# Optimization experiments

Measured on AMD Instinct MI355X. Metric: run time of the kernel, lower is better.

## Reference

```python
import jax, jax.numpy as jnp
from jax import lax
import numpy as np

# (mult_l0, mult_l1, mult_l2) per layer, from CNN.__init__
FEATS = [(5, 0, 0), (10, 3, 0), (10, 3, 1), (16, 8, 1), (16, 8, 1), (16, 8, 1), (1, 0, 0)]
STRIDES = [2, 1, 1, 1, 1, 1]
RELUS = [True, True, True, True, True, False]
SIZE, NRAD, PAD = 7, 3, 3  # SE3Convolution(size=7, n_radial=3, padding=3)


def ch(r):
    return r[0] + 3 * r[1] + 5 * r[2]


def radial_basis():
    # precomputed fixed radial shell basis on the 7^3 kernel grid (stand-in for
    # e3nn's precomputed spherical-harmonic x radial kernel basis)
    r = np.arange(SIZE) - SIZE // 2
    X, Y, Z = np.meshgrid(r, r, r, indexing='ij')
    dist = np.sqrt(X ** 2 + Y ** 2 + Z ** 2)
    centers = np.linspace(0.0, SIZE // 2, NRAD)
    sigma = (SIZE // 2) / (NRAD - 1)
    b = np.exp(-((dist[None] - centers[:, None, None, None]) ** 2) / (2.0 * sigma ** 2))
    return jnp.asarray(b, jnp.float32)  # [NRAD, 7, 7, 7]


def setup_inputs() -> dict:
    key = jax.random.key(0)
    ks = jax.random.split(key, 20)
    inp = {"x": jax.random.normal(ks[0], (2, 5, 32, 32, 32), jnp.float32)}
    for i in range(6):
        cin = ch(FEATS[i]) + 9 * FEATS[i][1]  # after TensorProduct concat
        cout = ch(FEATS[i + 1])
        inp[f"w{i}"] = jax.random.normal(ks[1 + i], (cout, cin, NRAD), jnp.float32) / np.sqrt(cin * SIZE ** 3)
    for i in range(5):
        inp[f"b{i}"] = jax.random.normal(ks[7 + i], (FEATS[i + 1][0],), jnp.float32) * 0.1
    inp["lin_w"] = jax.random.normal(ks[13], (1, 5), jnp.float32)
    inp["lin_b"] = jax.random.normal(ks[14], (1,), jnp.float32)
    inp["alpha"] = jnp.ones((1,), jnp.float32)
    return inp


def _block(x, w, bias, rep_in, rep_out, stride, relu, basis):
    m1, m3, m5 = rep_in
    B = x.shape[0]
    if m3 > 0:
        # TensorProduct on the l=1 fields: self outer product -> 3x3 (9-dim) fields
        sp = x.shape[2:]
        v = x[:, m1:m1 + 3 * m3].reshape(B, m3, 3, *sp)
        t = jnp.einsum('bmixyz,bmjxyz->bmijxyz', v, v).reshape(B, m3 * 9, *sp)
        x = jnp.concatenate([x, t], axis=1)
    # SE3Convolution: learned mixing of precomputed kernel basis, then conv3d
    k = jnp.einsum('oir,rxyz->oixyz', w, basis)  # [Cout, Cin, 7,7,7]
    x = lax.conv_general_dilated(x, k, (stride,) * 3, [(PAD, PAD)] * 3,
                                 dimension_numbers=('NCDHW', 'OIDHW', 'NCDHW'))
    if relu:
        n1, n3, n5 = rep_out
        sp = x.shape[2:]
        # SE3BatchNorm: per-field norm over batch + spatial (per multiplicity channel)
        parts, off = [], 0
        for m, d in ((n1, 1), (n3, 3), (n5, 5)):
            if m == 0:
                continue
            f = x[:, off:off + m * d].reshape(B, m, d, *sp)
            norm2 = jnp.mean(jnp.sum(f * f, axis=2), axis=(0, 2, 3, 4))  # [m]
            f = f / jnp.sqrt(norm2 + 1e-5)[None, :, None, None, None, None]
            parts.append(f.reshape(B, m * d, *sp))
            off += m * d
        x = jnp.concatenate(parts, axis=1)
        # BiasRelu: bias + relu on scalar (l=0) fields only, higher-l pass through
        s = jax.nn.relu(x[:, :n1] + bias[None, :, None, None, None])
        x = jnp.concatenate([s, x[:, n1:]], axis=1)
    return x


def reference(x, w0, w1, w2, w3, w4, w5, b0, b1, b2, b3, b4, lin_w, lin_b, alpha):
    basis = radial_basis()
    ws = [w0, w1, w2, w3, w4, w5]
    bs = [b0, b1, b2, b3, b4, None]
    inp = x
    for i in range(6):
        x = _block(x, ws[i], bs[i], FEATS[i], FEATS[i + 1], STRIDES[i], RELUS[i], basis)
    B = x.shape[0]
    out = x.reshape(B, x.shape[1], -1).mean(-1) * alpha * 0.1  # [B, 1]
    y = inp.reshape(B, 5, -1).sum(-1) @ lin_w.T + lin_b  # [B, 1]
    return out + y
```

## Files before the change

kernel.cpp:

```cpp
#include <hip/hip_runtime.h>
#include <math.h>

static constexpr int OFF_BAS = 0;
static constexpr int OFF_W   = 1280;
static constexpr int OFF_ACC = 37504;
static constexpr int OFF_XA  = 37888;
static constexpr int OFF_XB  = OFF_XA + 761856;
static constexpr int OFF_U   = OFF_XB + 761856;
static constexpr int OFF_Y   = OFF_U + 1105920;

static constexpr int WOFF0 = OFF_W + 0;
static constexpr int WOFF1 = OFF_W + 384;
static constexpr int WOFF2 = OFF_W + 3264;
static constexpr int WOFF3 = OFF_W + 9248;
static constexpr int WOFF4 = OFF_W + 22304;
static constexpr int WOFF5 = OFF_W + 35360;

__device__ __forceinline__ float wred(float s) {
  #pragma unroll
  for (int o = 32; o > 0; o >>= 1) s += __shfl_xor(s, o, 64);
  return s;
}

__global__ __launch_bounds__(128) void prep_kernel(
    const float* __restrict__ w0, const float* __restrict__ w1,
    const float* __restrict__ w2, const float* __restrict__ w3,
    const float* __restrict__ w4, const float* __restrict__ w5,
    float* __restrict__ ws) {
  const int blk = blockIdx.x;
  const int tid = threadIdx.x;
  if (blk == 0) {
    for (int i = tid; i < 1176; i += 128) {
      int tx = i & 7;
      int r  = (i >> 3) % 3;
      int ty = (i / 24) % 7;
      int tz = i / 168;
      float val = 0.f;
      if (tx < 7) {
        double dx = tx - 3, dy = ty - 3, dz = tz - 3;
        double dist = sqrt(dx * dx + dy * dy + dz * dz);
        double d = dist - 1.5 * (double)r;
        val = (float)exp(-(d * d) / 4.5);
      }
      ws[OFF_BAS + i] = val;
    }
    return;
  }
  const int row = blk - 1;
  const int rs[6]    = {0, 24, 96, 232, 368, 504};
  const int kk[6]    = {15, 37, 42, 93, 93, 93};
  const int k4[6]    = {16, 40, 44, 96, 96, 96};
  const int coutt[6] = {19, 24, 45, 45, 45, 1};
  const int cinf[6]  = {5, 46, 51, 117, 117, 117};
  const int chin_[6] = {5, 19, 24, 45, 45, 45};
  const int woff[6]  = {WOFF0, WOFF1, WOFF2, WOFF3, WOFF4, WOFF5};
  const float* wptr[6] = {w0, w1, w2, w3, w4, w5};
  int l = 0;
  while (l < 5 && row >= rs[l + 1]) ++l;
  const int m = row - rs[l];
  const int K = kk[l], K4 = k4[l];
  const float* w = wptr[l];
  float* Wo = ws + woff[l] + m * K4;
  if (l == 0) {
    for (int k = tid; k < 16; k += 128) {
      float v = 0.f;
      if (m < 19 && k < 15) { int c = k / 3, r = k % 3; v = w[(m * 5 + c) * 3 + r]; }
      Wo[k] = v;
    }
    return;
  }
  const int o = m / 3, r = m % 3;
  const int cout = coutt[l];
  const int cf = cinf[l], ch = chin_[l];
  const int itab[6] = {0, 0, 0, 1, 1, 2};
  const int jtab[6] = {0, 1, 2, 1, 2, 2};
  for (int k = tid; k < K4; k += 128) {
    float v = 0.f;
    if (o < cout && k < K) {
      if (k < ch) {
        v = w[(o * cf + k) * 3 + r];
      } else {
        int cc = k - ch;
        int mm = cc / 6, uu = cc % 6;
        int i = itab[uu], j = jtab[uu];
        v = w[(o * cf + ch + mm * 9 + i * 3 + j) * 3 + r];
        if (i != j) v += w[(o * cf + ch + mm * 9 + j * 3 + i) * 3 + r];
      }
    }
    Wo[k] = v;
  }
}

__global__ __launch_bounds__(256) void insum_kernel(const float* __restrict__ x,
                                                    float* __restrict__ insum) {
  const int g = blockIdx.x * 256 + threadIdx.x;
  float4 v = ((const float4*)x)[g];
  float s = v.x + v.y + v.z + v.w;
  s = wred(s);
  if ((threadIdx.x & 63) == 0) atomicAdd(&insum[g >> 13], s);
}

__global__ __launch_bounds__(256) void dw0_kernel(const float* __restrict__ x,
                                                  const float* __restrict__ basg,
                                                  float* __restrict__ z0) {
  const int g = blockIdx.x * 256 + threadIdx.x;
  const int p = g & 4095;
  const int c = (g >> 12) % 5;
  const int b = g / (5 * 4096);
  const int X = p & 15, Y = (p >> 4) & 15, Z = p >> 8;
  const float* xp = x + (((size_t)(b * 5 + c)) << 15);
  float a0 = 0.f, a1 = 0.f, a2 = 0.f;
  for (int tz = 0; tz < 7; ++tz) {
    const int iz = 2 * Z + tz - 3;
    if ((unsigned)iz >= 32u) continue;
    for (int ty = 0; ty < 7; ++ty) {
      const int iy = 2 * Y + ty - 3;
      if ((unsigned)iy >= 32u) continue;
      const float* bb = &basg[(tz * 7 + ty) * 24];
      const float* row = xp + (iz << 10) + (iy << 5);
      #pragma unroll
      for (int tx = 0; tx < 7; ++tx) {
        const int ix = 2 * X + tx - 3;
        float v = ((unsigned)ix < 32u) ? row[ix] : 0.f;
        a0 = fmaf(bb[tx], v, a0);
        a1 = fmaf(bb[8 + tx], v, a1);
        a2 = fmaf(bb[16 + tx], v, a2);
      }
    }
  }
  const size_t base = (((size_t)(b * 15 + c * 3)) << 12) + p;
  z0[base] = a0;
  z0[base + 4096] = a1;
  z0[base + 8192] = a2;
}

template <int K>
__global__ __launch_bounds__(256) void gemm_kernel(
    const float* __restrict__ in, const float* __restrict__ W,
    float* __restrict__ out, int Mreal, float* __restrict__ chsum) {
  constexpr int K4 = (K + 3) & ~3;
  __shared__ float Wl[8 * K4];
  const int b = blockIdx.z;
  const int m0 = blockIdx.y * 8;
  const int p0 = blockIdx.x * 1024 + threadIdx.x * 4;
  for (int i = threadIdx.x; i < 8 * K4; i += 256) Wl[i] = W[m0 * K4 + i];
  __syncthreads();
  const float* ip = in + (((size_t)b * K) << 12) + p0;
  float4 acc[8];
  #pragma unroll
  for (int j = 0; j < 8; ++j) acc[j] = make_float4(0.f, 0.f, 0.f, 0.f);
  int k = 0;
  for (; k + 4 <= K; k += 4) {
    const float4 v0 = *(const float4*)&ip[(size_t)(k + 0) << 12];
    const float4 v1 = *(const float4*)&ip[(size_t)(k + 1) << 12];
    const float4 v2 = *(const float4*)&ip[(size_t)(k + 2) << 12];
    const float4 v3 = *(const float4*)&ip[(size_t)(k + 3) << 12];
    #pragma unroll
    for (int j = 0; j < 8; ++j) {
      const float4 wv = *(const float4*)&Wl[j * K4 + k];
      acc[j].x = fmaf(wv.x, v0.x, acc[j].x); acc[j].y = fmaf(wv.x, v0.y, acc[j].y);
      acc[j].z = fmaf(wv.x, v0.z, acc[j].z); acc[j].w = fmaf(wv.x, v0.w, acc[j].w);
      acc[j].x = fmaf(wv.y, v1.x, acc[j].x); acc[j].y = fmaf(wv.y, v1.y, acc[j].y);
      acc[j].z = fmaf(wv.y, v1.z, acc[j].z); acc[j].w = fmaf(wv.y, v1.w, acc[j].w);
      acc[j].x = fmaf(wv.z, v2.x, acc[j].x); acc[j].y = fmaf(wv.z, v2.y, acc[j].y);
      acc[j].z = fmaf(wv.z, v2.z, acc[j].z); acc[j].w = fmaf(wv.z, v2.w, acc[j].w);
      acc[j].x = fmaf(wv.w, v3.x, acc[j].x); acc[j].y = fmaf(wv.w, v3.y, acc[j].y);
      acc[j].z = fmaf(wv.w, v3.z, acc[j].z); acc[j].w = fmaf(wv.w, v3.w, acc[j].w);
    }
  }
  for (; k < K; ++k) {
    const float4 v = *(const float4*)&ip[(size_t)k << 12];
    #pragma unroll
    for (int j = 0; j < 8; ++j) {
      const float w = Wl[j * K4 + k];
      acc[j].x = fmaf(w, v.x, acc[j].x); acc[j].y = fmaf(w, v.y, acc[j].y);
      acc[j].z = fmaf(w, v.z, acc[j].z); acc[j].w = fmaf(w, v.w, acc[j].w);
    }
  }
  #pragma unroll
  for (int j = 0; j < 8; ++j) {
    const int m = m0 + j;
    if (m < Mreal) *(float4*)&out[(((size_t)(b * Mreal + m)) << 12) + p0] = acc[j];
  }
  if (chsum) {
    #pragma unroll
    for (int j = 0; j < 8; ++j) {
      float s = acc[j].x * acc[j].x + acc[j].y * acc[j].y +
                acc[j].z * acc[j].z + acc[j].w * acc[j].w;
      s = wred(s);
      if ((threadIdx.x & 63) == 0) atomicAdd(&chsum[m0 + j], s);
    }
  }
}

__global__ __launch_bounds__(128) void dwB_kernel(
    const float* __restrict__ u, const float* __restrict__ basg,
    float* __restrict__ y, float* __restrict__ chsum, int cout) {
  __shared__ float lin[13440];
  const int b = blockIdx.y;
  const int o = blockIdx.x >> 3;
  const int rem = blockIdx.x & 7;
  const int zs = rem >> 1, yh = rem & 1;
  const int z0 = zs * 4, y0 = yh * 8;
  const int tid = threadIdx.x;
  const float* ubase = u + (((size_t)(b * 3 * cout + o * 3)) << 12);
  for (int i = tid; i < 3360; i += 128) {
    const int g = i & 7;
    const int row = i >> 3;
    const int ch = row / 140;
    const int rr = row - ch * 140;
    const int dz = rr / 14;
    const int dy = rr - dz * 14;
    const int gz = z0 + dz - 3, gy = y0 + dy - 3;
    float4 v = make_float4(0.f, 0.f, 0.f, 0.f);
    if (g >= 1 && g <= 4 && (unsigned)gz < 16u && (unsigned)gy < 16u)
      v = *(const float4*)&ubase[(ch << 12) + (gz << 8) + (gy << 4) + ((g - 1) << 2)];
    *(float4*)&lin[row * 32 + ((g ^ (row & 7)) << 2)] = v;
  }
  __syncthreads();
  const int yy = tid & 7, bx = (tid >> 3) & 3, zz = tid >> 5;
  float acc[4] = {0.f, 0.f, 0.f, 0.f};
  #pragma unroll 1
  for (int tz = 0; tz < 7; ++tz) {
    #pragma unroll 1
    for (int ty = 0; ty < 7; ++ty) {
      const int rbase = (zz + tz) * 14 + (yy + ty);
      const float* bbrow = &basg[(tz * 7 + ty) * 24];
      #pragma unroll
      for (int ch = 0; ch < 3; ++ch) {
        const int row = ch * 140 + rbase;
        const int s = row & 7;
        const int base = row * 32;
        const float4 v0 = *(const float4*)&lin[base + (((bx + 0) ^ s) << 2)];
        const float4 v1 = *(const float4*)&lin[base + (((bx + 1) ^ s) << 2)];
        const float4 v2 = *(const float4*)&lin[base + (((bx + 2) ^ s) << 2)];
        const float w_[12] = {v0.x, v0.y, v0.z, v0.w, v1.x, v1.y, v1.z, v1.w,
                              v2.x, v2.y, v2.z, v2.w};
        const float* bb = bbrow + ch * 8;
        #pragma unroll
        for (int tx = 0; tx < 7; ++tx) {
          const float w = bb[tx];
          #pragma unroll
          for (int i2 = 0; i2 < 4; ++i2)
            acc[i2] = fmaf(w, w_[i2 + tx + 1], acc[i2]);
        }
      }
    }
  }
  const int p = ((z0 + zz) << 8) + ((y0 + yy) << 4) + bx * 4;
  float4 outv = {acc[0], acc[1], acc[2], acc[3]};
  *(float4*)&y[(((size_t)(b * cout + o)) << 12) + p] = outv;
  if (chsum) {
    float s = acc[0]*acc[0] + acc[1]*acc[1] + acc[2]*acc[2] + acc[3]*acc[3];
    s = wred(s);
    if ((tid & 63) == 0) atomicAdd(&chsum[o], s);
  }
}

template <int COUT, int N1, int N3>
__global__ __launch_bounds__(64) void post_kernel(
    const float* __restrict__ y, const float* __restrict__ chsum,
    const float* __restrict__ bias, float* __restrict__ xout) {
  constexpr int N5 = (COUT - N1 - 3 * N3) / 5;
  constexpr int CO = COUT + 6 * N3;
  const int b = blockIdx.y;
  const int p = blockIdx.x * 64 + threadIdx.x;
  const float* yp = y + (((size_t)b * COUT) << 12) + p;
  float* xp = xout + (((size_t)b * CO) << 12) + p;
  const float inv = 1.f / 8192.f;
  float vals[COUT];
  #pragma unroll
  for (int c = 0; c < N1; ++c) {
    const float f = 1.f / sqrtf(chsum[c] * inv + 1e-5f);
    const float v = yp[(size_t)c << 12] * f + bias[c];
    vals[c] = v > 0.f ? v : 0.f;
  }
  #pragma unroll
  for (int m = 0; m < N3; ++m) {
    const int c0 = N1 + 3 * m;
    const float f = 1.f / sqrtf((chsum[c0] + chsum[c0 + 1] + chsum[c0 + 2]) * inv + 1e-5f);
    vals[c0]     = yp[(size_t)c0 << 12] * f;
    vals[c0 + 1] = yp[(size_t)(c0 + 1) << 12] * f;
    vals[c0 + 2] = yp[(size_t)(c0 + 2) << 12] * f;
  }
  #pragma unroll
  for (int m = 0; m < N5; ++m) {
    const int c0 = N1 + 3 * N3 + 5 * m;
    const float s5 = chsum[c0] + chsum[c0+1] + chsum[c0+2] + chsum[c0+3] + chsum[c0+4];
    const float f = 1.f / sqrtf(s5 * inv + 1e-5f);
    #pragma unroll
    for (int d = 0; d < 5; ++d) vals[c0 + d] = yp[(size_t)(c0 + d) << 12] * f;
  }
  #pragma unroll
  for (int c = 0; c < COUT; ++c) xp[(size_t)c << 12] = vals[c];
  #pragma unroll
  for (int m = 0; m < N3; ++m) {
    const float v0 = vals[N1 + 3*m], v1 = vals[N1 + 3*m + 1], v2 = vals[N1 + 3*m + 2];
    const float t[6] = {v0*v0, v0*v1, v0*v2, v1*v1, v1*v2, v2*v2};
    #pragma unroll
    for (int uu = 0; uu < 6; ++uu) xp[(size_t)(COUT + m * 6 + uu) << 12] = t[uu];
  }
}

__global__ __launch_bounds__(256) void final_kernel(
    const float* __restrict__ y5, const float* __restrict__ acc,
    const float* __restrict__ lin_w, const float* __restrict__ lin_b,
    const float* __restrict__ alpha, float* __restrict__ out) {
  const int b = blockIdx.x;
  const int tid = threadIdx.x;
  float s = 0.f;
  for (int i = tid; i < 4096; i += 256) s += y5[(b << 12) + i];
  s = wred(s);
  __shared__ float ls[4];
  if ((tid & 63) == 0) ls[tid >> 6] = s;
  __syncthreads();
  if (tid == 0) {
    const float t = ls[0] + ls[1] + ls[2] + ls[3];
    float res = t * (1.f / 4096.f) * alpha[0] * 0.1f;
    const float* insum = acc + 240;
    for (int c = 0; c < 5; ++c) res += insum[b * 5 + c] * lin_w[c];
    res += lin_b[0];
    out[b] = res;
  }
}

extern "C" void kernel_launch(void* const* d_in, const int* in_sizes, int n_in,
                              void* d_out, int out_size, void* d_ws, size_t ws_size,
                              hipStream_t stream) {
  const float* x  = (const float*)d_in[0];
  const float* w0 = (const float*)d_in[1];
  const float* w1 = (const float*)d_in[2];
  const float* w2 = (const float*)d_in[3];
  const float* w3 = (const float*)d_in[4];
  const float* w4 = (const float*)d_in[5];
  const float* w5 = (const float*)d_in[6];
  const float* b0 = (const float*)d_in[7];
  const float* b1 = (const float*)d_in[8];
  const float* b2 = (const float*)d_in[9];
  const float* b3 = (const float*)d_in[10];
  const float* b4 = (const float*)d_in[11];
  const float* lw = (const float*)d_in[12];
  const float* lb = (const float*)d_in[13];
  const float* al = (const float*)d_in[14];
  float* out = (float*)d_out;
  float* ws = (float*)d_ws;

  float* bas = ws + OFF_BAS;
  float* acc = ws + OFF_ACC;
  float* XA = ws + OFF_XA;
  float* XB = ws + OFF_XB;
  float* U  = ws + OFF_U;
  float* Y  = ws + OFF_Y;

  hipMemsetAsync(acc, 0, 256 * sizeof(float), stream);
  hipLaunchKernelGGL(prep_kernel, dim3(513), dim3(128), 0, stream, w0, w1, w2, w3, w4, w5, ws);
  hipLaunchKernelGGL(insum_kernel, dim3(320), dim3(256), 0, stream, x, acc + 240);

  hipLaunchKernelGGL(dw0_kernel, dim3(160), dim3(256), 0, stream, x, bas, U);
  hipLaunchKernelGGL(gemm_kernel<15>, dim3(4, 3, 2), dim3(256), 0, stream,
                     U, ws + WOFF0, Y, 19, acc);
  hipLaunchKernelGGL((post_kernel<19, 10, 3>), dim3(64, 2), dim3(64), 0, stream, Y, acc, b0, XA);

  hipLaunchKernelGGL(gemm_kernel<37>, dim3(4, 9, 2), dim3(256), 0, stream,
                     XA, ws + WOFF1, U, 72, (float*)nullptr);
  hipLaunchKernelGGL(dwB_kernel, dim3(192, 2), dim3(128), 0, stream, U, bas, Y, acc + 48, 24);
  hipLaunchKernelGGL((post_kernel<24, 10, 3>), dim3(64, 2), dim3(64), 0, stream, Y, acc + 48, b1, XB);

  hipLaunchKernelGGL(gemm_kernel<42>, dim3(4, 17, 2), dim3(256), 0, stream,
                     XB, ws + WOFF2, U, 135, (float*)nullptr);
  hipLaunchKernelGGL(dwB_kernel, dim3(360, 2), dim3(128), 0, stream, U, bas, Y, acc + 96, 45);
  hipLaunchKernelGGL((post_kernel<45, 16, 8>), dim3(64, 2), dim3(64), 0, stream, Y, acc + 96, b2, XA);

  hipLaunchKernelGGL(gemm_kernel<93>, dim3(4, 17, 2), dim3(256), 0, stream,
                     XA, ws + WOFF3, U, 135, (float*)nullptr);
  hipLaunchKernelGGL(dwB_kernel, dim3(360, 2), dim3(128), 0, stream, U, bas, Y, acc + 144, 45);
  hipLaunchKernelGGL((post_kernel<45, 16, 8>), dim3(64, 2), dim3(64), 0, stream, Y, acc + 144, b3, XB);

  hipLaunchKernelGGL(gemm_kernel<93>, dim3(4, 17, 2), dim3(256), 0, stream,
                     XB, ws + WOFF4, U, 135, (float*)nullptr);
  hipLaunchKernelGGL(dwB_kernel, dim3(360, 2), dim3(128), 0, stream, U, bas, Y, acc + 192, 45);
  hipLaunchKernelGGL((post_kernel<45, 16, 8>), dim3(64, 2), dim3(64), 0, stream, Y, acc + 192, b4, XA);

  hipLaunchKernelGGL(gemm_kernel<93>, dim3(4, 1, 2), dim3(256), 0, stream,
                     XA, ws + WOFF5, U, 3, (float*)nullptr);
  hipLaunchKernelGGL(dwB_kernel, dim3(8, 2), dim3(128), 0, stream, U, bas, Y, (float*)nullptr, 1);

  hipLaunchKernelGGL(final_kernel, dim3(2), dim3(256), 0, stream, Y, acc, lw, lb, al, out);
}
```

Baseline: 450.9 us.

## Compact LDS layout and double-buffer shared-memory loads in depthwise conv kernel

Shrinks the padded shared-memory tile from 8 to 6 float4 per row and drops the XOR swizzle, so less LDS is allocated and filled per block. The 7x7 (tz,ty) loop is flattened into 49 iterations with two register buffers, so LDS reads for the next tap row are issued while FMAs for the current one run. This raises register pressure and may bring back LDS bank conflicts without the swizzle. It also unrolls the fill loop.

```diff
diff --git a/kernel.cpp b/kernel.cpp
--- a/kernel.cpp
+++ b/kernel.cpp
@@ -196,7 +196,7 @@
 __global__ __launch_bounds__(128) void dwB_kernel(
     const float* __restrict__ u, const float* __restrict__ basg,
     float* __restrict__ y, float* __restrict__ chsum, int cout) {
-  __shared__ float lin[13440];
+  __shared__ float lin[11760];
   const int b = blockIdx.y;
   const int o = blockIdx.x >> 3;
   const int rem = blockIdx.x & 7;
@@ -204,9 +204,10 @@
   const int z0 = zs * 4, y0 = yh * 8;
   const int tid = threadIdx.x;
   const float* ubase = u + (((size_t)(b * 3 * cout + o * 3)) << 12);
-  for (int i = tid; i < 3360; i += 128) {
-    const int g = i & 7;
-    const int row = i >> 3;
+  #pragma unroll 5
+  for (int i = tid; i < 2520; i += 128) {
+    const int row = i / 6;
+    const int g = i - row * 6;
     const int ch = row / 140;
     const int rr = row - ch * 140;
     const int dz = rr / 14;
@@ -215,38 +216,48 @@
     float4 v = make_float4(0.f, 0.f, 0.f, 0.f);
     if (g >= 1 && g <= 4 && (unsigned)gz < 16u && (unsigned)gy < 16u)
       v = *(const float4*)&ubase[(ch << 12) + (gz << 8) + (gy << 4) + ((g - 1) << 2)];
-    *(float4*)&lin[row * 32 + ((g ^ (row & 7)) << 2)] = v;
+    *(float4*)&lin[row * 28 + (g << 2)] = v;
   }
   __syncthreads();
   const int yy = tid & 7, bx = (tid >> 3) & 3, zz = tid >> 5;
   float acc[4] = {0.f, 0.f, 0.f, 0.f};
-  #pragma unroll 1
-  for (int tz = 0; tz < 7; ++tz) {
-    #pragma unroll 1
-    for (int ty = 0; ty < 7; ++ty) {
-      const int rbase = (zz + tz) * 14 + (yy + ty);
-      const float* bbrow = &basg[(tz * 7 + ty) * 24];
+  float4 PA[9], PB[9];
+  auto LOADSET = [&](float4* P, int it) {
+    const int tz = it / 7;
+    const int ty = it - tz * 7;
+    const int rbase = ((zz + tz) * 14 + (yy + ty)) * 28 + (bx << 2);
+    #pragma unroll
+    for (int ch = 0; ch < 3; ++ch) {
       #pragma unroll
-      for (int ch = 0; ch < 3; ++ch) {
-        const int row = ch * 140 + rbase;
-        const int s = row & 7;
-        const int base = row * 32;
-        const float4 v0 = *(const float4*)&lin[base + (((bx + 0) ^ s) << 2)];
-        const float4 v1 = *(const float4*)&lin[base + (((bx + 1) ^ s) << 2)];
-        const float4 v2 = *(const float4*)&lin[base + (((bx + 2) ^ s) << 2)];
-        const float w_[12] = {v0.x, v0.y, v0.z, v0.w, v1.x, v1.y, v1.z, v1.w,
-                              v2.x, v2.y, v2.z, v2.w};
-        const float* bb = bbrow + ch * 8;
+      for (int k = 0; k < 3; ++k)
+        P[ch * 3 + k] = *(const float4*)&lin[rbase + ch * 3920 + (k << 2)];
+    }
+  };
+  auto COMPSET = [&](const float4* P, int it) {
+    const float* bb = &basg[it * 24];
+    #pragma unroll
+    for (int ch = 0; ch < 3; ++ch) {
+      #pragma unroll
+      for (int tx = 0; tx < 7; ++tx) {
+        const float w = bb[ch * 8 + tx];
         #pragma unroll
-        for (int tx = 0; tx < 7; ++tx) {
-          const float w = bb[tx];
-          #pragma unroll
-          for (int i2 = 0; i2 < 4; ++i2)
-            acc[i2] = fmaf(w, w_[i2 + tx + 1], acc[i2]);
+        for (int i2 = 0; i2 < 4; ++i2) {
+          const int j = i2 + tx + 1;
+          acc[i2] = fmaf(w, ((const float*)&P[ch * 3 + (j >> 2)])[j & 3], acc[i2]);
         }
       }
     }
-  }
+  };
+  LOADSET(PA, 0);
+  #pragma unroll 1
+  for (int itp = 0; itp < 24; ++itp) {
+    const int it = itp * 2;
+    LOADSET(PB, it + 1);
+    COMPSET(PA, it);
+    LOADSET(PA, it + 2);
+    COMPSET(PB, it + 1);
+  }
+  COMPSET(PA, 48);
   const int p = ((z0 + zz) << 8) + ((y0 + yy) << 4) + bx * 4;
   float4 outv = {acc[0], acc[1], acc[2], acc[3]};
   *(float4*)&y[(((size_t)(b * cout + o)) << 12) + p] = outv;
```

New measurement: 488.1 us. 1.08x slower.
